# Performance work log

Hardware: AMD Instinct MI355X
Metric: run time of the kernel (lower is better)

Reference implementation:

```python
import jax, jax.numpy as jnp
from jax import lax
import numpy as np

FEAT_STRIDE = 16
PRE_NMS_TOP_N = 2000
POST_NMS_TOP_N = 300
NMS_THRESH = 0.7


def _whctrs(a):
    w = a[2] - a[0] + 1.0
    h = a[3] - a[1] + 1.0
    return w, h, a[0] + 0.5 * (w - 1.0), a[1] + 0.5 * (h - 1.0)


def _mkanchors(ws, hs, x_ctr, y_ctr):
    ws = np.asarray(ws, dtype=np.float64)
    hs = np.asarray(hs, dtype=np.float64)
    return np.stack([x_ctr - 0.5 * (ws - 1.0), y_ctr - 0.5 * (hs - 1.0),
                     x_ctr + 0.5 * (ws - 1.0), y_ctr + 0.5 * (hs - 1.0)], axis=1)


def generate_anchors(base_size=16, ratios=np.array([0.5, 1.0, 2.0]), scales=np.array([8.0, 16.0, 32.0])):
    base = np.array([1.0, 1.0, float(base_size), float(base_size)]) - 1.0
    w, h, xc, yc = _whctrs(base)
    size = w * h
    ws = np.round(np.sqrt(size / ratios))
    hs = np.round(ws * ratios)
    ratio_anchors = _mkanchors(ws, hs, xc, yc)
    out = []
    for i in range(ratio_anchors.shape[0]):
        w_i, h_i, xc_i, yc_i = _whctrs(ratio_anchors[i])
        out.append(_mkanchors(w_i * scales, h_i * scales, xc_i, yc_i))
    return np.vstack(out).astype(np.float32)


ANCHORS = generate_anchors()  # [A=9, 4]
NUM_ANCHORS = ANCHORS.shape[0]


def _nms_keep(boxes, thresh):
    # boxes [N,4], already sorted by descending score; torchvision IoU convention.
    x1, y1, x2, y2 = boxes[:, 0], boxes[:, 1], boxes[:, 2], boxes[:, 3]
    areas = (x2 - x1) * (y2 - y1)
    xx1 = jnp.maximum(x1[:, None], x1[None, :])
    yy1 = jnp.maximum(y1[:, None], y1[None, :])
    xx2 = jnp.minimum(x2[:, None], x2[None, :])
    yy2 = jnp.minimum(y2[:, None], y2[None, :])
    inter = jnp.clip(xx2 - xx1, 0.0) * jnp.clip(yy2 - yy1, 0.0)
    iou = inter / (areas[:, None] + areas[None, :] - inter + 1e-9)
    n = boxes.shape[0]
    # sup[i, j] True => box i (higher score) suppresses later box j
    sup = (iou > thresh) & jnp.triu(jnp.ones((n, n), bool), 1)

    def body(i, keep):
        return keep & ~(keep[i] & sup[i])

    return lax.fori_loop(0, n, body, jnp.ones((n,), bool))


def setup_inputs() -> dict:
    key = jax.random.key(0)
    k1, k2 = jax.random.split(key)
    B, A, H, W = 8, NUM_ANCHORS, 128, 128
    scores = jax.random.normal(k1, (B, 2 * A, H, W), jnp.float32)
    bbox_deltas = jax.random.normal(k2, (B, 4 * A, H, W), jnp.float32) * 0.2
    im_h = float(H * FEAT_STRIDE)
    im_w = float(W * FEAT_STRIDE)
    im_info = jnp.tile(jnp.array([[im_h, im_w, 1.0]], jnp.float32), (B, 1))
    return {"scores": scores, "bbox_deltas": bbox_deltas, "im_info": im_info}


def reference(scores, bbox_deltas, im_info):
    B, _, H, W = scores.shape
    A = NUM_ANCHORS
    # --- anchor generation over the feature grid ---
    sx = jnp.arange(W, dtype=jnp.float32) * FEAT_STRIDE
    sy = jnp.arange(H, dtype=jnp.float32) * FEAT_STRIDE
    gx, gy = jnp.meshgrid(sx, sy)  # 'xy' indexing matches np.meshgrid default
    shifts = jnp.stack([gx.ravel(), gy.ravel(), gx.ravel(), gy.ravel()], axis=1)  # [K,4]
    anchors = (jnp.asarray(ANCHORS)[None, :, :] + shifts[:, None, :]).reshape(-1, 4)  # [K*A,4]

    obj_scores = scores[:, A:].transpose(0, 2, 3, 1).reshape(B, -1)   # [B, K*A]
    deltas = bbox_deltas.transpose(0, 2, 3, 1).reshape(B, -1, 4)      # [B, K*A, 4]

    # --- bbox_transform_inv ---
    widths = anchors[:, 2] - anchors[:, 0] + 1.0
    heights = anchors[:, 3] - anchors[:, 1] + 1.0
    ctr_x = anchors[:, 0] + 0.5 * widths
    ctr_y = anchors[:, 1] + 0.5 * heights
    dx, dy, dw, dh = deltas[..., 0], deltas[..., 1], deltas[..., 2], deltas[..., 3]
    pred_ctr_x = dx * widths + ctr_x
    pred_ctr_y = dy * heights + ctr_y
    pred_w = jnp.exp(dw) * widths
    pred_h = jnp.exp(dh) * heights
    proposals = jnp.stack([pred_ctr_x - 0.5 * pred_w, pred_ctr_y - 0.5 * pred_h,
                           pred_ctr_x + 0.5 * pred_w, pred_ctr_y + 0.5 * pred_h], axis=-1)

    # --- clip_boxes: im_info[b] = (h, w, scale) ---
    max_x = (im_info[:, 1] - 1.0)[:, None]
    max_y = (im_info[:, 0] - 1.0)[:, None]
    proposals = jnp.stack([
        jnp.clip(proposals[..., 0], 0.0, max_x),
        jnp.clip(proposals[..., 1], 0.0, max_y),
        jnp.clip(proposals[..., 2], 0.0, max_x),
        jnp.clip(proposals[..., 3], 0.0, max_y)], axis=-1)

    # --- pre-NMS top-k by score ---
    _, order = lax.top_k(obj_scores, PRE_NMS_TOP_N)                  # [B, pre]
    top_props = jnp.take_along_axis(proposals, order[..., None], axis=1)  # [B, pre, 4]

    # --- per-image greedy NMS (fixed-size, jit-compatible) ---
    keep = jax.vmap(lambda b: _nms_keep(b, NMS_THRESH))(top_props)   # [B, pre] bool
    sel = jnp.argsort(jnp.where(keep, 0, 1), axis=1, stable=True)[:, :POST_NMS_TOP_N]
    valid = jnp.take_along_axis(keep, sel, axis=1)                   # [B, post]
    out_boxes = jnp.take_along_axis(top_props, sel[..., None], axis=1) * valid[..., None].astype(top_props.dtype)

    batch_idx = jnp.broadcast_to(
        jnp.arange(B, dtype=out_boxes.dtype)[:, None, None], (B, POST_NMS_TOP_N, 1))
    return jnp.concatenate([batch_idx, out_boxes], axis=-1)  # [B, post_nms_topN, 5]
```

## Files before the change

kernel.cpp:

```cpp
#include <hip/hip_runtime.h>

#define NB 8
#define NA 9
#define HH 128
#define WW 128
#define NCELL (HH * WW)
#define NTOT (NCELL * NA)
#define PRE_K 2000
#define POST_K 300
#define CAP 4096
#define HBLK 18
#define NMS_TH 0.7f

__constant__ float c_aw[NA] = {184.f, 368.f, 736.f, 128.f, 256.f, 512.f, 88.f, 176.f, 352.f};
__constant__ float c_ah[NA] = {96.f, 192.f, 384.f, 128.f, 256.f, 512.f, 176.f, 352.f, 704.f};

__device__ __forceinline__ unsigned int sortable(float s) {
    unsigned int u = __float_as_uint(s);
    return (u & 0x80000000u) ? ~u : (u | 0x80000000u);
}

__device__ __forceinline__ unsigned long long shflx64(unsigned long long v, int m) {
    return __shfl_xor(v, m, 64);
}

__global__ __launch_bounds__(1024) void hist0_kernel(const float* __restrict__ scores,
                                                     unsigned int* __restrict__ h0out) {
    __shared__ unsigned int h[2048];
    int b = blockIdx.y, tid = threadIdx.x;
    h[tid] = 0; h[tid + 1024] = 0;
    __syncthreads();
    const float4* sp4 = (const float4*)(scores + (size_t)b * 18 * NCELL + (size_t)NA * NCELL);
    int base4 = blockIdx.x * 2048;
#pragma unroll
    for (int e = 0; e < 2; ++e) {
        float4 v = sp4[base4 + e * 1024 + tid];
        atomicAdd(&h[sortable(v.x) >> 21], 1u);
        atomicAdd(&h[sortable(v.y) >> 21], 1u);
        atomicAdd(&h[sortable(v.z) >> 21], 1u);
        atomicAdd(&h[sortable(v.w) >> 21], 1u);
    }
    __syncthreads();
    unsigned int* o = h0out + ((size_t)(b * HBLK + blockIdx.x)) * 2048;
    o[tid] = h[tid];
    o[tid + 1024] = h[tid + 1024];
}

__global__ __launch_bounds__(1024) void select0_kernel(const unsigned int* __restrict__ h0out,
                                                       uint2* __restrict__ state0) {
    __shared__ unsigned int thr[1024];
    int b = blockIdx.x, tid = threadIdx.x;
    unsigned int c0 = 0, c1 = 0;
    for (int p = 0; p < HBLK; ++p) {
        const unsigned int* hp = h0out + ((size_t)(b * HBLK + p)) * 2048;
        uint2 v = *(const uint2*)&hp[2 * tid];
        c0 += v.x; c1 += v.y;
    }
    thr[tid] = c0 + c1;
    __syncthreads();
    for (int off = 1; off < 1024; off <<= 1) {
        unsigned int v = (tid + off < 1024) ? thr[tid + off] : 0u;
        __syncthreads();
        thr[tid] += v;
        __syncthreads();
    }
    unsigned int above = (tid < 1023) ? thr[tid + 1] : 0u;
    if (thr[tid] >= (unsigned)PRE_K && above < (unsigned)PRE_K) {
        if (above + c1 >= (unsigned)PRE_K)
            state0[b] = make_uint2((unsigned)(2 * tid + 1), (unsigned)(PRE_K)-above);
        else
            state0[b] = make_uint2((unsigned)(2 * tid), (unsigned)(PRE_K)-above - c1);
    }
}

__global__ __launch_bounds__(1024) void hist1_kernel(const float* __restrict__ scores,
                                                     const uint2* __restrict__ state0,
                                                     unsigned int* __restrict__ gh1) {
    __shared__ unsigned int h[128];
    int b = blockIdx.y, tid = threadIdx.x;
    if (tid < 128) h[tid] = 0;
    __syncthreads();
    unsigned int piv = state0[b].x;
    const float4* sp4 = (const float4*)(scores + (size_t)b * 18 * NCELL + (size_t)NA * NCELL);
    int base4 = blockIdx.x * 2048;
#pragma unroll
    for (int e = 0; e < 2; ++e) {
        float4 v = sp4[base4 + e * 1024 + tid];
        unsigned int u;
        u = sortable(v.x); if ((u >> 21) == piv) atomicAdd(&h[(u >> 14) & 127u], 1u);
        u = sortable(v.y); if ((u >> 21) == piv) atomicAdd(&h[(u >> 14) & 127u], 1u);
        u = sortable(v.z); if ((u >> 21) == piv) atomicAdd(&h[(u >> 14) & 127u], 1u);
        u = sortable(v.w); if ((u >> 21) == piv) atomicAdd(&h[(u >> 14) & 127u], 1u);
    }
    __syncthreads();
    if (tid < 128 && h[tid]) atomicAdd(&gh1[b * 128 + tid], h[tid]);
}

__global__ void select1_kernel(const unsigned int* __restrict__ gh1,
                               const uint2* __restrict__ state0,
                               unsigned int* __restrict__ state1) {
    int b = blockIdx.x, lane = threadIdx.x;
    unsigned int c0 = 0, c1 = 0;
    if (lane < 64) {
        c0 = gh1[b * 128 + 2 * lane];
        c1 = gh1[b * 128 + 2 * lane + 1];
    }
    unsigned int sum = c0 + c1;
#pragma unroll
    for (int off = 1; off < 64; off <<= 1) {
        unsigned int v = __shfl_down(sum, off, 64);
        if (lane + off < 64) sum += v;
    }
    unsigned int above = __shfl_down(sum, 1, 64);
    if (lane == 63) above = 0;
    unsigned int need0 = state0[b].y;
    if (sum >= need0 && above < need0) {
        unsigned int d = (above + c1 >= need0) ? (unsigned)(2 * lane + 1) : (unsigned)(2 * lane);
        unsigned int prefix = (state0[b].x << 7) | d;
        state1[b] = prefix << 14;
    }
}

__global__ void gather_kernel(const float* __restrict__ scores,
                              const unsigned int* __restrict__ state1,
                              int* __restrict__ cnt,
                              unsigned long long* __restrict__ buf) {
    __shared__ unsigned long long lbuf[2048];
    __shared__ int lcnt;
    __shared__ int gbase;
    int b = blockIdx.y;
    int tid = threadIdx.x;
    if (tid == 0) lcnt = 0;
    __syncthreads();
    unsigned int P = state1[b];
    const float4* sp4 = (const float4*)(scores + (size_t)b * 18 * NCELL + (size_t)NA * NCELL);
    int base4 = blockIdx.x * 512;
#pragma unroll
    for (int e = 0; e < 2; ++e) {
        int t4 = base4 + e * 256 + tid;
        float4 v = sp4[t4];
        float el[4] = {v.x, v.y, v.z, v.w};
#pragma unroll
        for (int j = 0; j < 4; ++j) {
            unsigned int u = sortable(el[j]);
            if (u >= P) {
                int idx4 = t4 * 4 + j;
                int a = idx4 >> 14;
                int cell = idx4 & 16383;
                unsigned int i = (unsigned int)cell * 9u + (unsigned int)a;
                int pos = atomicAdd(&lcnt, 1);
                lbuf[pos] = ((unsigned long long)u << 32) |
                            (unsigned long long)(0xFFFFFFFFu - i);
            }
        }
    }
    __syncthreads();
    if (tid == 0) gbase = atomicAdd(&cnt[b], lcnt);
    __syncthreads();
    int m = lcnt, gb = gbase;
    for (int t = tid; t < m; t += 256) {
        int g = gb + t;
        if (g < CAP) buf[(size_t)b * CAP + g] = lbuf[t];
    }
}

#define SHFL_STEP(J)                                                          \
    {                                                                         \
        int d_ = (J) >> 1;                                                    \
        bool keepMax = (((tid & d_) == 0) == (((2u * (unsigned)tid) & k) == 0)); \
        unsigned long long pa = shflx64(va, d_);                              \
        unsigned long long pb = shflx64(vb, d_);                              \
        va = keepMax ? (va > pa ? va : pa) : (va < pa ? va : pa);             \
        vb = keepMax ? (vb > pb ? vb : pb) : (vb < pb ? vb : pb);             \
    }
#define LOCAL_STEP()                                                          \
    {                                                                         \
        bool desc = (((2u * (unsigned)tid) & k) == 0);                        \
        unsigned long long lo = va < vb ? va : vb;                            \
        unsigned long long hi = va < vb ? vb : va;                            \
        va = desc ? hi : lo; vb = desc ? lo : hi;                             \
    }

__global__ __launch_bounds__(1024) void sort_kernel(const unsigned long long* __restrict__ buf,
                                                    const int* __restrict__ cnt,
                                                    unsigned int* __restrict__ topidx) {
    __shared__ unsigned long long s[CAP];
    int b = blockIdx.x;
    int tid = threadIdx.x;
    int n = min(cnt[b], CAP);
    const unsigned long long* src = buf + (size_t)b * CAP;
    if (n <= 2048) {
        unsigned long long va = (2 * tid < n) ? src[2 * tid] : 0ULL;
        unsigned long long vb = (2 * tid + 1 < n) ? src[2 * tid + 1] : 0ULL;
#pragma unroll
        for (unsigned k = 2; k <= 128; k <<= 1) {
#pragma unroll
            for (unsigned j = k >> 1; j >= 2; j >>= 1) SHFL_STEP(j)
            LOCAL_STEP()
        }
        for (unsigned k = 256; k <= 2048; k <<= 1) {
            s[2 * tid] = va; s[2 * tid + 1] = vb;
            __syncthreads();
            for (unsigned j = k >> 1; j >= 128; j >>= 1) {
                for (int t = tid; t < 2048; t += 1024) {
                    int ixj = t ^ (int)j;
                    if (ixj > t) {
                        unsigned long long x = s[t], y = s[ixj];
                        if ((((unsigned)t & k) == 0) ? (x < y) : (x > y)) { s[t] = y; s[ixj] = x; }
                    }
                }
                __syncthreads();
            }
            va = s[2 * tid]; vb = s[2 * tid + 1];
#pragma unroll
            for (unsigned j = 64; j >= 2; j >>= 1) SHFL_STEP(j)
            LOCAL_STEP()
        }
        s[2 * tid] = va; s[2 * tid + 1] = vb;
        __syncthreads();
    } else {
        for (int t = tid; t < CAP; t += 1024)
            s[t] = (t < n) ? src[t] : 0ULL;
        __syncthreads();
        for (int k = 2; k <= CAP; k <<= 1) {
            for (int j = k >> 1; j > 0; j >>= 1) {
                for (int t = tid; t < CAP; t += 1024) {
                    int ixj = t ^ j;
                    if (ixj > t) {
                        unsigned long long x = s[t], y = s[ixj];
                        if (((t & k) == 0) ? (x < y) : (x > y)) { s[t] = y; s[ixj] = x; }
                    }
                }
                __syncthreads();
            }
        }
    }
    for (int r = tid; r < PRE_K; r += 1024)
        topidx[(size_t)b * PRE_K + r] = 0xFFFFFFFFu - (unsigned int)(s[r] & 0xFFFFFFFFu);
}

__global__ void decode_kernel(const unsigned int* __restrict__ topidx,
                              const float* __restrict__ deltas,
                              const float* __restrict__ im_info,
                              float4* __restrict__ props) {
    int gid = blockIdx.x * 256 + threadIdx.x;
    if (gid >= NB * PRE_K) return;
    int b = gid / PRE_K;
    unsigned int i = topidx[gid];
    unsigned int cell = i / 9u;
    unsigned int a = i - cell * 9u;
    int wx = (int)(cell & 127u), hy = (int)(cell >> 7);
    const float* dp = deltas + (size_t)b * 36 * NCELL + (size_t)(4u * a) * NCELL +
                      (size_t)hy * WW + wx;
    float dx = dp[0];
    float dy = dp[NCELL];
    float dw = dp[2 * NCELL];
    float dh = dp[3 * NCELL];
    float W_ = c_aw[a], H_ = c_ah[a];
    float cx = (float)(16 * wx + 8), cy = (float)(16 * hy + 8);
    float px = __fadd_rn(__fmul_rn(dx, W_), cx);
    float py = __fadd_rn(__fmul_rn(dy, H_), cy);
    float pw = __fmul_rn((float)exp((double)dw), W_);
    float ph = __fmul_rn((float)exp((double)dh), H_);
    float hw = __fmul_rn(0.5f, pw), hh = __fmul_rn(0.5f, ph);
    float x1 = __fsub_rn(px, hw), y1 = __fsub_rn(py, hh);
    float x2 = __fadd_rn(px, hw), y2 = __fadd_rn(py, hh);
    float maxx = __fsub_rn(im_info[b * 3 + 1], 1.0f);
    float maxy = __fsub_rn(im_info[b * 3 + 0], 1.0f);
    x1 = fminf(fmaxf(x1, 0.0f), maxx);
    y1 = fminf(fmaxf(y1, 0.0f), maxy);
    x2 = fminf(fmaxf(x2, 0.0f), maxx);
    y2 = fminf(fmaxf(y2, 0.0f), maxy);
    props[gid] = make_float4(x1, y1, x2, y2);
}

__global__ void mask_kernel(const float4* __restrict__ boxes,
                            unsigned long long* __restrict__ mask) {
    int colB = blockIdx.x, rowB = blockIdx.y, b = blockIdx.z;
    if (colB < rowB) return;
    __shared__ float4 cb[64];
    int t = threadIdx.x;
    int j0 = colB * 64;
    cb[t] = (j0 + t < PRE_K) ? boxes[(size_t)b * PRE_K + j0 + t] : make_float4(0.f, 0.f, -1.f, -1.f);
    __syncthreads();
    int i = rowB * 64 + t;
    if (i >= PRE_K) return;
    float4 mb = boxes[(size_t)b * PRE_K + i];
    float aarea = __fmul_rn(__fsub_rn(mb.z, mb.x), __fsub_rn(mb.w, mb.y));
    unsigned long long m = 0ULL;
    for (int jj = 0; jj < 64; ++jj) {
        int j = j0 + jj;
        if (j > i && j < PRE_K) {
            float4 c = cb[jj];
            float xx1 = fmaxf(mb.x, c.x), yy1 = fmaxf(mb.y, c.y);
            float xx2 = fminf(mb.z, c.z), yy2 = fminf(mb.w, c.w);
            float iw = fmaxf(__fsub_rn(xx2, xx1), 0.0f);
            float ih = fmaxf(__fsub_rn(yy2, yy1), 0.0f);
            float inter = __fmul_rn(iw, ih);
            float barea = __fmul_rn(__fsub_rn(c.z, c.x), __fsub_rn(c.w, c.y));
            float denom = __fadd_rn(__fsub_rn(__fadd_rn(aarea, barea), inter), 1e-9f);
            float iou = __fdiv_rn(inter, denom);
            if (iou > NMS_TH) m |= (1ULL << jj);
        }
    }
    mask[((size_t)(b * PRE_K + i)) * 32 + colB] = m;
}

#define CH 16
#define NCH (PRE_K / CH)

#define LOAD_CHUNK(BUF, C)                                               \
    _Pragma("unroll") for (int t = 0; t < CH; ++t) BUF[t] =              \
        act ? mrow[((size_t)((C) * CH + t)) * 32 + lane] : 0ULL;

#define PROCESS_CHUNK(BUF, CBASE)                                        \
    {                                                                    \
        int w = (CBASE) >> 6;                                            \
        unsigned long long rw = __shfl(remv, w, 64);                     \
        _Pragma("unroll") for (int t = 0; t < CH; ++t) {                 \
            int i = (CBASE) + t;                                         \
            if (!((rw >> (i & 63)) & 1ULL)) {                            \
                if (lane == 0 && cnt < POST_K) keeplist[cnt] = i;        \
                cnt++;                                                   \
                if (lane >= w) remv |= BUF[t];                           \
                rw |= __shfl(BUF[t], w, 64);                             \
            }                                                            \
        }                                                                \
    }

__global__ void scan_kernel(const unsigned long long* __restrict__ mask,
                            const float4* __restrict__ boxes,
                            float* __restrict__ out) {
    int b = blockIdx.x;
    int lane = threadIdx.x;
    const unsigned long long* mrow = mask + (size_t)b * PRE_K * 32;
    __shared__ int keeplist[POST_K];
    bool act = lane < 32;
    unsigned long long remv = 0ULL;
    int cnt = 0;
    unsigned long long bufA[CH], bufB[CH], bufC[CH];
    LOAD_CHUNK(bufA, 0)
    LOAD_CHUNK(bufB, 1)
    LOAD_CHUNK(bufC, 2)
    for (int c = 0; c < NCH; c += 3) {
        PROCESS_CHUNK(bufA, c * CH)
        if (cnt >= POST_K) break;
        if (c + 3 < NCH) { LOAD_CHUNK(bufA, c + 3) }
        if (c + 1 < NCH) {
            PROCESS_CHUNK(bufB, (c + 1) * CH)
            if (cnt >= POST_K) break;
            if (c + 4 < NCH) { LOAD_CHUNK(bufB, c + 4) }
        }
        if (c + 2 < NCH) {
            PROCESS_CHUNK(bufC, (c + 2) * CH)
            if (cnt >= POST_K) break;
            if (c + 5 < NCH) { LOAD_CHUNK(bufC, c + 5) }
        }
    }
    __syncthreads();
    int K = min(cnt, POST_K);
    const float4* bb = boxes + (size_t)b * PRE_K;
    for (int r = lane; r < POST_K; r += 64) {
        float4 v = make_float4(0.f, 0.f, 0.f, 0.f);
        if (r < K) v = bb[keeplist[r]];
        float* o = out + ((size_t)b * POST_K + r) * 5;
        o[0] = (float)b;
        o[1] = v.x;
        o[2] = v.y;
        o[3] = v.z;
        o[4] = v.w;
    }
}

extern "C" void kernel_launch(void* const* d_in, const int* in_sizes, int n_in,
                              void* d_out, int out_size, void* d_ws, size_t ws_size,
                              hipStream_t stream) {
    const float* scores = (const float*)d_in[0];
    const float* deltas = (const float*)d_in[1];
    const float* im_info = (const float*)d_in[2];
    float* out = (float*)d_out;
    char* ws = (char*)d_ws;

    unsigned int* h0out = (unsigned int*)(ws + 0);
    unsigned int* gh1 = (unsigned int*)(ws + 1179648);
    uint2* state0 = (uint2*)(ws + 1183744);
    unsigned int* state1 = (unsigned int*)(ws + 1183808);
    int* cnt = (int*)(ws + 1183872);
    unsigned long long* buf = (unsigned long long*)(ws + 1183936);
    unsigned int* topidx = (unsigned int*)(ws + 1446080);
    float4* props = (float4*)(ws + 1510080);
    unsigned long long* mask = (unsigned long long*)(ws + 1766080);

    hipMemsetAsync(ws + 1179648, 0, 4288, stream);
    hipLaunchKernelGGL(hist0_kernel, dim3(HBLK, NB), dim3(1024), 0, stream, scores, h0out);
    hipLaunchKernelGGL(select0_kernel, dim3(NB), dim3(1024), 0, stream, h0out, state0);
    hipLaunchKernelGGL(hist1_kernel, dim3(HBLK, NB), dim3(1024), 0, stream, scores, state0, gh1);
    hipLaunchKernelGGL(select1_kernel, dim3(NB), dim3(64), 0, stream, gh1, state0, state1);
    hipLaunchKernelGGL(gather_kernel, dim3(72, NB), dim3(256), 0, stream, scores, state1, cnt, buf);
    hipLaunchKernelGGL(sort_kernel, dim3(NB), dim3(1024), 0, stream, buf, cnt, topidx);
    hipLaunchKernelGGL(decode_kernel, dim3((NB * PRE_K + 255) / 256), dim3(256), 0, stream,
                       topidx, deltas, im_info, props);
    hipLaunchKernelGGL(mask_kernel, dim3(32, 32, NB), dim3(64), 0, stream, props, mask);
    hipLaunchKernelGGL(scan_kernel, dim3(NB), dim3(64), 0, stream, mask, props, out);
}
```

Baseline: 120.6 us.

## Rewrite NMS as column-major mask with block-parallel wavefront scan, fold memset

The suppression mask is stored column-major per 64-box tile, so each box j holds bits for which earlier boxes in tile iT suppress it. The scan now processes 64 boxes at a time. Each lane ORs the masks of the previously kept words to decide whether it is still alive, then resolves suppression inside the tile with ballots. This replaces the serial per-box chunked scan. Separately, the histogram kernels use half as many blocks, each doing twice the loads, and the workspace memset is folded into select0_kernel, which removes one API call. The risks are more global reads per tile in the scan (quadratic in tile index) and less parallelism in the histogram passes.

```diff
diff --git a/kernel.cpp b/kernel.cpp
--- a/kernel.cpp
+++ b/kernel.cpp
@@ -9,7 +9,7 @@
 #define PRE_K 2000
 #define POST_K 300
 #define CAP 4096
-#define HBLK 18
+#define HBLK 9
 #define NMS_TH 0.7f
 
 __constant__ float c_aw[NA] = {184.f, 368.f, 736.f, 128.f, 256.f, 512.f, 88.f, 176.f, 352.f};
@@ -31,9 +31,9 @@
     h[tid] = 0; h[tid + 1024] = 0;
     __syncthreads();
     const float4* sp4 = (const float4*)(scores + (size_t)b * 18 * NCELL + (size_t)NA * NCELL);
-    int base4 = blockIdx.x * 2048;
-#pragma unroll
-    for (int e = 0; e < 2; ++e) {
+    int base4 = blockIdx.x * 4096;
+#pragma unroll
+    for (int e = 0; e < 4; ++e) {
         float4 v = sp4[base4 + e * 1024 + tid];
         atomicAdd(&h[sortable(v.x) >> 21], 1u);
         atomicAdd(&h[sortable(v.y) >> 21], 1u);
@@ -47,9 +47,13 @@
 }
 
 __global__ __launch_bounds__(1024) void select0_kernel(const unsigned int* __restrict__ h0out,
-                                                       uint2* __restrict__ state0) {
+                                                       uint2* __restrict__ state0,
+                                                       unsigned int* __restrict__ gh1,
+                                                       int* __restrict__ cnt) {
     __shared__ unsigned int thr[1024];
     int b = blockIdx.x, tid = threadIdx.x;
+    if (tid < 128) gh1[b * 128 + tid] = 0;
+    if (tid == 0) cnt[b] = 0;
     unsigned int c0 = 0, c1 = 0;
     for (int p = 0; p < HBLK; ++p) {
         const unsigned int* hp = h0out + ((size_t)(b * HBLK + p)) * 2048;
@@ -82,9 +86,9 @@
     __syncthreads();
     unsigned int piv = state0[b].x;
     const float4* sp4 = (const float4*)(scores + (size_t)b * 18 * NCELL + (size_t)NA * NCELL);
-    int base4 = blockIdx.x * 2048;
-#pragma unroll
-    for (int e = 0; e < 2; ++e) {
+    int base4 = blockIdx.x * 4096;
+#pragma unroll
+    for (int e = 0; e < 4; ++e) {
         float4 v = sp4[base4 + e * 1024 + tid];
         unsigned int u;
         u = sortable(v.x); if ((u >> 21) == piv) atomicAdd(&h[(u >> 14) & 127u], 1u);
@@ -275,90 +279,78 @@
 }
 
 __global__ void mask_kernel(const float4* __restrict__ boxes,
-                            unsigned long long* __restrict__ mask) {
-    int colB = blockIdx.x, rowB = blockIdx.y, b = blockIdx.z;
-    if (colB < rowB) return;
-    __shared__ float4 cb[64];
+                            unsigned long long* __restrict__ colm) {
+    int iT = blockIdx.x, jT = blockIdx.y, b = blockIdx.z;
+    if (iT > jT) return;
+    __shared__ float4 ib[64];
     int t = threadIdx.x;
-    int j0 = colB * 64;
-    cb[t] = (j0 + t < PRE_K) ? boxes[(size_t)b * PRE_K + j0 + t] : make_float4(0.f, 0.f, -1.f, -1.f);
-    __syncthreads();
-    int i = rowB * 64 + t;
-    if (i >= PRE_K) return;
-    float4 mb = boxes[(size_t)b * PRE_K + i];
-    float aarea = __fmul_rn(__fsub_rn(mb.z, mb.x), __fsub_rn(mb.w, mb.y));
+    int i0 = iT * 64;
+    ib[t] = (i0 + t < PRE_K) ? boxes[(size_t)b * PRE_K + i0 + t] : make_float4(0.f, 0.f, -1.f, -1.f);
+    __syncthreads();
+    int j = jT * 64 + t;
+    if (j >= PRE_K) return;
+    float4 jb = boxes[(size_t)b * PRE_K + j];
+    float barea = __fmul_rn(__fsub_rn(jb.z, jb.x), __fsub_rn(jb.w, jb.y));
     unsigned long long m = 0ULL;
-    for (int jj = 0; jj < 64; ++jj) {
-        int j = j0 + jj;
-        if (j > i && j < PRE_K) {
-            float4 c = cb[jj];
-            float xx1 = fmaxf(mb.x, c.x), yy1 = fmaxf(mb.y, c.y);
-            float xx2 = fminf(mb.z, c.z), yy2 = fminf(mb.w, c.w);
+    for (int ii = 0; ii < 64; ++ii) {
+        int i = i0 + ii;
+        if (i < j) {
+            float4 c = ib[ii];
+            float aarea = __fmul_rn(__fsub_rn(c.z, c.x), __fsub_rn(c.w, c.y));
+            float xx1 = fmaxf(c.x, jb.x), yy1 = fmaxf(c.y, jb.y);
+            float xx2 = fminf(c.z, jb.z), yy2 = fminf(c.w, jb.w);
             float iw = fmaxf(__fsub_rn(xx2, xx1), 0.0f);
             float ih = fmaxf(__fsub_rn(yy2, yy1), 0.0f);
             float inter = __fmul_rn(iw, ih);
-            float barea = __fmul_rn(__fsub_rn(c.z, c.x), __fsub_rn(c.w, c.y));
             float denom = __fadd_rn(__fsub_rn(__fadd_rn(aarea, barea), inter), 1e-9f);
             float iou = __fdiv_rn(inter, denom);
-            if (iou > NMS_TH) m |= (1ULL << jj);
-        }
-    }
-    mask[((size_t)(b * PRE_K + i)) * 32 + colB] = m;
-}
-
-#define CH 16
-#define NCH (PRE_K / CH)
-
-#define LOAD_CHUNK(BUF, C)                                               \
-    _Pragma("unroll") for (int t = 0; t < CH; ++t) BUF[t] =              \
-        act ? mrow[((size_t)((C) * CH + t)) * 32 + lane] : 0ULL;
-
-#define PROCESS_CHUNK(BUF, CBASE)                                        \
-    {                                                                    \
-        int w = (CBASE) >> 6;                                            \
-        unsigned long long rw = __shfl(remv, w, 64);                     \
-        _Pragma("unroll") for (int t = 0; t < CH; ++t) {                 \
-            int i = (CBASE) + t;                                         \
-            if (!((rw >> (i & 63)) & 1ULL)) {                            \
-                if (lane == 0 && cnt < POST_K) keeplist[cnt] = i;        \
-                cnt++;                                                   \
-                if (lane >= w) remv |= BUF[t];                           \
-                rw |= __shfl(BUF[t], w, 64);                             \
-            }                                                            \
-        }                                                                \
-    }
-
-__global__ void scan_kernel(const unsigned long long* __restrict__ mask,
+            if (iou > NMS_TH) m |= (1ULL << ii);
+        }
+    }
+    colm[((size_t)b * 32 + iT) * 2048 + j] = m;
+}
+
+__global__ void scan_kernel(const unsigned long long* __restrict__ colm,
                             const float4* __restrict__ boxes,
                             float* __restrict__ out) {
     int b = blockIdx.x;
     int lane = threadIdx.x;
-    const unsigned long long* mrow = mask + (size_t)b * PRE_K * 32;
+    __shared__ unsigned long long kw[32];
     __shared__ int keeplist[POST_K];
-    bool act = lane < 32;
-    unsigned long long remv = 0ULL;
-    int cnt = 0;
-    unsigned long long bufA[CH], bufB[CH], bufC[CH];
-    LOAD_CHUNK(bufA, 0)
-    LOAD_CHUNK(bufB, 1)
-    LOAD_CHUNK(bufC, 2)
-    for (int c = 0; c < NCH; c += 3) {
-        PROCESS_CHUNK(bufA, c * CH)
-        if (cnt >= POST_K) break;
-        if (c + 3 < NCH) { LOAD_CHUNK(bufA, c + 3) }
-        if (c + 1 < NCH) {
-            PROCESS_CHUNK(bufB, (c + 1) * CH)
-            if (cnt >= POST_K) break;
-            if (c + 4 < NCH) { LOAD_CHUNK(bufB, c + 4) }
-        }
-        if (c + 2 < NCH) {
-            PROCESS_CHUNK(bufC, (c + 2) * CH)
-            if (cnt >= POST_K) break;
-            if (c + 5 < NCH) { LOAD_CHUNK(bufC, c + 5) }
-        }
-    }
-    __syncthreads();
-    int K = min(cnt, POST_K);
+    const unsigned long long* cb = colm + (size_t)b * 32 * 2048;
+    int total = 0;
+    bool done = false;
+    for (int k = 0; k < 32 && !done; ++k) {
+        int j = k * 64 + lane;
+        unsigned long long d = 0;
+        int w = 0;
+        for (; w + 4 <= k; w += 4) {
+            unsigned long long a0 = cb[(size_t)(w + 0) * 2048 + j] & kw[w + 0];
+            unsigned long long a1 = cb[(size_t)(w + 1) * 2048 + j] & kw[w + 1];
+            unsigned long long a2 = cb[(size_t)(w + 2) * 2048 + j] & kw[w + 2];
+            unsigned long long a3 = cb[(size_t)(w + 3) * 2048 + j] & kw[w + 3];
+            d |= (a0 | a1) | (a2 | a3);
+        }
+        for (; w < k; ++w) d |= cb[(size_t)w * 2048 + j] & kw[w];
+        unsigned long long diag = cb[(size_t)k * 2048 + j];
+        bool alive_me = (d == 0ULL) && (j < PRE_K);
+        unsigned long long alive = __ballot(alive_me);
+        unsigned long long keptw = 0ULL;
+        while (alive) {
+            int i = __builtin_ctzll(alive);
+            keptw |= (1ULL << i);
+            if (lane == 0) keeplist[total] = k * 64 + i;
+            total++;
+            if (total >= POST_K) { done = true; break; }
+            unsigned long long sup = __ballot(((diag >> i) & 1ULL) != 0ULL);
+            alive &= ~sup;
+            alive &= ~keptw;
+        }
+        if (lane == 0) kw[k] = keptw;
+        __syncthreads();
+    }
+    __syncthreads();
+    int K = min(total, POST_K);
     const float4* bb = boxes + (size_t)b * PRE_K;
     for (int r = lane; r < POST_K; r += 64) {
         float4 v = make_float4(0.f, 0.f, 0.f, 0.f);
@@ -382,24 +374,23 @@
     char* ws = (char*)d_ws;
 
     unsigned int* h0out = (unsigned int*)(ws + 0);
-    unsigned int* gh1 = (unsigned int*)(ws + 1179648);
-    uint2* state0 = (uint2*)(ws + 1183744);
-    unsigned int* state1 = (unsigned int*)(ws + 1183808);
-    int* cnt = (int*)(ws + 1183872);
-    unsigned long long* buf = (unsigned long long*)(ws + 1183936);
-    unsigned int* topidx = (unsigned int*)(ws + 1446080);
-    float4* props = (float4*)(ws + 1510080);
-    unsigned long long* mask = (unsigned long long*)(ws + 1766080);
-
-    hipMemsetAsync(ws + 1179648, 0, 4288, stream);
+    unsigned int* gh1 = (unsigned int*)(ws + 589824);
+    uint2* state0 = (uint2*)(ws + 593920);
+    unsigned int* state1 = (unsigned int*)(ws + 593984);
+    int* cnt = (int*)(ws + 594048);
+    unsigned long long* buf = (unsigned long long*)(ws + 594112);
+    unsigned int* topidx = (unsigned int*)(ws + 856256);
+    float4* props = (float4*)(ws + 920256);
+    unsigned long long* colm = (unsigned long long*)(ws + 1176320);
+
     hipLaunchKernelGGL(hist0_kernel, dim3(HBLK, NB), dim3(1024), 0, stream, scores, h0out);
-    hipLaunchKernelGGL(select0_kernel, dim3(NB), dim3(1024), 0, stream, h0out, state0);
+    hipLaunchKernelGGL(select0_kernel, dim3(NB), dim3(1024), 0, stream, h0out, state0, gh1, cnt);
     hipLaunchKernelGGL(hist1_kernel, dim3(HBLK, NB), dim3(1024), 0, stream, scores, state0, gh1);
     hipLaunchKernelGGL(select1_kernel, dim3(NB), dim3(64), 0, stream, gh1, state0, state1);
     hipLaunchKernelGGL(gather_kernel, dim3(72, NB), dim3(256), 0, stream, scores, state1, cnt, buf);
     hipLaunchKernelGGL(sort_kernel, dim3(NB), dim3(1024), 0, stream, buf, cnt, topidx);
     hipLaunchKernelGGL(decode_kernel, dim3((NB * PRE_K + 255) / 256), dim3(256), 0, stream,
                        topidx, deltas, im_info, props);
-    hipLaunchKernelGGL(mask_kernel, dim3(32, 32, NB), dim3(64), 0, stream, props, mask);
-    hipLaunchKernelGGL(scan_kernel, dim3(NB), dim3(64), 0, stream, mask, props, out);
-}
+    hipLaunchKernelGGL(mask_kernel, dim3(32, 32, NB), dim3(64), 0, stream, props, colm);
+    hipLaunchKernelGGL(scan_kernel, dim3(NB), dim3(64), 0, stream, colm, props, out);
+}
```

Measured after the change: 106.1 us. 12.0% less time.
